# Optimization experiments

Hardware: AMD Instinct MI355X
Metric: run time of the kernel (lower is better)

Reference implementation:

```python
import jax, jax.numpy as jnp
import numpy as np

WEIGHT1 = 0.5
WEIGHT2 = 0.5
COS_EPS = 1e-8  # F.cosine_similarity default eps


def setup_inputs() -> dict:
    key = jax.random.key(0)
    k1, k2, k3 = jax.random.split(key, 3)
    B, D, C = 65536, 512, 1000
    x = jax.random.normal(k1, (B, D), dtype=jnp.float32)
    label = jax.random.randint(k2, (B,), 0, C)
    global_prototype = jax.random.normal(k3, (C, D), dtype=jnp.float32)
    return {"x": x, "label": label, "global_prototype": global_prototype}


def reference(x, label, global_prototype):
    # Batched prototype gather: [B, D]
    protos = global_prototype[label]
    # Per-row MSE (mean over feature dim), matching F.mse_loss per sample
    diff = x - protos
    edu_dist = jnp.mean(diff * diff, axis=1)  # [B]
    # Per-row cosine distance: 1 - dot / max(||x||*||p||, eps)
    dot = jnp.sum(x * protos, axis=1)
    nx = jnp.sqrt(jnp.sum(x * x, axis=1))
    npn = jnp.sqrt(jnp.sum(protos * protos, axis=1))
    cos = dot / jnp.maximum(nx * npn, COS_EPS)
    cos_dist = 1.0 - cos  # [B]
    loss = WEIGHT1 * jnp.mean(edu_dist) + WEIGHT2 * jnp.mean(cos_dist)
    return loss
```

## Files before the change

### kernel.cpp

```cpp
#include <hip/hip_runtime.h>


constexpr int D_DIM = 512;
constexpr float COS_EPS = 1e-8f;
constexpr int NBLOCKS = 2048;

__global__ __launch_bounds__(256) void proto_loss_partial(
    const float* __restrict__ x,
    const int* __restrict__ label,
    const float* __restrict__ proto,
    float* __restrict__ partials,
    int B)
{
    const int lane = threadIdx.x & 63;
    const int wave = threadIdx.x >> 6;
    const int wavesPerBlock = blockDim.x >> 6;
    const int gwave = blockIdx.x * wavesPerBlock + wave;
    const int nwaves = gridDim.x * wavesPerBlock;

    float acc = 0.0f;
    for (int row = gwave; row < B; row += nwaves) {
        const float4* __restrict__ xr =
            reinterpret_cast<const float4*>(x + (size_t)row * D_DIM);
        const int lbl = label[row];
        const float4* __restrict__ pr =
            reinterpret_cast<const float4*>(proto + (size_t)lbl * D_DIM);

        float4 x0 = xr[lane];
        float4 p0 = pr[lane];
        float4 x1 = xr[lane + 64];
        float4 p1 = pr[lane + 64];

        float dot = x0.x*p0.x + x0.y*p0.y + x0.z*p0.z + x0.w*p0.w
                  + x1.x*p1.x + x1.y*p1.y + x1.z*p1.z + x1.w*p1.w;
        float sx  = x0.x*x0.x + x0.y*x0.y + x0.z*x0.z + x0.w*x0.w
                  + x1.x*x1.x + x1.y*x1.y + x1.z*x1.z + x1.w*x1.w;
        float sp  = p0.x*p0.x + p0.y*p0.y + p0.z*p0.z + p0.w*p0.w
                  + p1.x*p1.x + p1.y*p1.y + p1.z*p1.z + p1.w*p1.w;

        #pragma unroll
        for (int off = 32; off > 0; off >>= 1) {
            dot += __shfl_down(dot, off, 64);
            sx  += __shfl_down(sx,  off, 64);
            sp  += __shfl_down(sp,  off, 64);
        }

        if (lane == 0) {
            float sse   = sx - 2.0f*dot + sp;
            float denom = fmaxf(sqrtf(sx) * sqrtf(sp), COS_EPS);
            float cosv  = dot / denom;
            acc += 0.5f * (sse * (1.0f / D_DIM)) + 0.5f * (1.0f - cosv);
        }
    }

    __shared__ float smem[8];
    if (lane == 0) smem[wave] = acc;
    __syncthreads();
    if (threadIdx.x == 0) {
        float s = 0.0f;
        for (int w = 0; w < wavesPerBlock; ++w) s += smem[w];
        partials[blockIdx.x] = s;
    }
}

__global__ __launch_bounds__(1024) void proto_loss_final(
    const float* __restrict__ partials, int n, float invB,
    float* __restrict__ out)
{
    __shared__ float smem[16];
    const int lane = threadIdx.x & 63;
    const int wave = threadIdx.x >> 6;

    float v = 0.0f;
    for (int i = threadIdx.x; i < n; i += blockDim.x) v += partials[i];

    #pragma unroll
    for (int off = 32; off > 0; off >>= 1) v += __shfl_down(v, off, 64);

    if (lane == 0) smem[wave] = v;
    __syncthreads();
    if (threadIdx.x == 0) {
        float s = 0.0f;
        const int nw = blockDim.x >> 6;
        for (int w = 0; w < nw; ++w) s += smem[w];
        out[0] = s * invB;
    }
}

extern "C" void kernel_launch(void* const* d_in, const int* in_sizes, int n_in,
                              void* d_out, int out_size, void* d_ws, size_t ws_size,
                              hipStream_t stream) {
    const float* x     = (const float*)d_in[0];
    const int*   label = (const int*)d_in[1];
    const float* proto = (const float*)d_in[2];
    float* out = (float*)d_out;
    float* partials = (float*)d_ws;

    const int B = in_sizes[1];

    proto_loss_partial<<<NBLOCKS, 256, 0, stream>>>(x, label, proto, partials, B);
    proto_loss_final<<<1, 1024, 0, stream>>>(partials, NBLOCKS, 1.0f / (float)B, out);
}
```

Before: 194.3 us.

## Process four rows per wave with 16-lane groups and contiguous row chunks

Each wave now splits into four 16-lane groups, and each group handles its own row, loading 8 float4 per operand per lane instead of 2. The shuffle reduction shrinks to 4 steps within a group. Rows are given to waves as contiguous blocks rather than strided, and per-lane accumulators are reduced across the wave at the end. The goal is more loads in flight per lane and fewer shuffle steps per row, at the cost of more registers and a load pattern where each group touches a different row.

Result: no change. 194.1 us (-0.1%).

```diff
diff --git a/kernel.cpp b/kernel.cpp
--- a/kernel.cpp
+++ b/kernel.cpp
@@ -1,9 +1,12 @@
 #include <hip/hip_runtime.h>
 
 
-constexpr int D_DIM = 512;
+constexpr int D_DIM   = 512;
 constexpr float COS_EPS = 1e-8f;
 constexpr int NBLOCKS = 2048;
+constexpr int G       = 16;
+constexpr int F4      = (D_DIM / 4) / G;
+constexpr int RPP     = 64 / G;
 
 __global__ __launch_bounds__(256) void proto_loss_partial(
     const float* __restrict__ x,
@@ -14,44 +17,53 @@
 {
     const int lane = threadIdx.x & 63;
     const int wave = threadIdx.x >> 6;
+    const int sub  = lane & (G - 1);
+    const int grp  = lane >> 4;
     const int wavesPerBlock = blockDim.x >> 6;
-    const int gwave = blockIdx.x * wavesPerBlock + wave;
+    const int gwave  = blockIdx.x * wavesPerBlock + wave;
     const int nwaves = gridDim.x * wavesPerBlock;
 
+    const int rowsPerWave = (B + nwaves - 1) / nwaves;
+    const int base = gwave * rowsPerWave;
+
     float acc = 0.0f;
-    for (int row = gwave; row < B; row += nwaves) {
-        const float4* __restrict__ xr =
-            reinterpret_cast<const float4*>(x + (size_t)row * D_DIM);
-        const int lbl = label[row];
-        const float4* __restrict__ pr =
-            reinterpret_cast<const float4*>(proto + (size_t)lbl * D_DIM);
 
-        float4 x0 = xr[lane];
-        float4 p0 = pr[lane];
-        float4 x1 = xr[lane + 64];
-        float4 p1 = pr[lane + 64];
+    for (int r0 = 0; r0 < rowsPerWave; r0 += RPP) {
+        const int row = base + r0 + grp;
+        if (row < B) {
+            const int lbl = label[row];
+            const float4* __restrict__ xr =
+                reinterpret_cast<const float4*>(x + (size_t)row * D_DIM);
+            const float4* __restrict__ pr =
+                reinterpret_cast<const float4*>(proto + (size_t)lbl * D_DIM);
 
-        float dot = x0.x*p0.x + x0.y*p0.y + x0.z*p0.z + x0.w*p0.w
-                  + x1.x*p1.x + x1.y*p1.y + x1.z*p1.z + x1.w*p1.w;
-        float sx  = x0.x*x0.x + x0.y*x0.y + x0.z*x0.z + x0.w*x0.w
-                  + x1.x*x1.x + x1.y*x1.y + x1.z*x1.z + x1.w*x1.w;
-        float sp  = p0.x*p0.x + p0.y*p0.y + p0.z*p0.z + p0.w*p0.w
-                  + p1.x*p1.x + p1.y*p1.y + p1.z*p1.z + p1.w*p1.w;
+            float dot = 0.0f, sx = 0.0f, sp = 0.0f;
+            #pragma unroll
+            for (int k = 0; k < F4; ++k) {
+                float4 xv = xr[sub + k * G];
+                float4 pv = pr[sub + k * G];
+                dot += xv.x*pv.x + xv.y*pv.y + xv.z*pv.z + xv.w*pv.w;
+                sx  += xv.x*xv.x + xv.y*xv.y + xv.z*xv.z + xv.w*xv.w;
+                sp  += pv.x*pv.x + pv.y*pv.y + pv.z*pv.z + pv.w*pv.w;
+            }
 
-        #pragma unroll
-        for (int off = 32; off > 0; off >>= 1) {
-            dot += __shfl_down(dot, off, 64);
-            sx  += __shfl_down(sx,  off, 64);
-            sp  += __shfl_down(sp,  off, 64);
-        }
+            #pragma unroll
+            for (int off = G / 2; off > 0; off >>= 1) {
+                dot += __shfl_down(dot, off, G);
+                sx  += __shfl_down(sx,  off, G);
+                sp  += __shfl_down(sp,  off, G);
+            }
 
-        if (lane == 0) {
-            float sse   = sx - 2.0f*dot + sp;
-            float denom = fmaxf(sqrtf(sx) * sqrtf(sp), COS_EPS);
-            float cosv  = dot / denom;
-            acc += 0.5f * (sse * (1.0f / D_DIM)) + 0.5f * (1.0f - cosv);
+            if (sub == 0) {
+                float sse   = sx - 2.0f * dot + sp;
+                float denom = fmaxf(sqrtf(sx) * sqrtf(sp), COS_EPS);
+                acc += 0.5f * (sse * (1.0f / D_DIM)) + 0.5f * (1.0f - dot / denom);
+            }
         }
     }
+
+    #pragma unroll
+    for (int off = 32; off > 0; off >>= 1) acc += __shfl_down(acc, off, 64);
 
     __shared__ float smem[8];
     if (lane == 0) smem[wave] = acc;
```
